# Optimization experiments

Measured on AMD Instinct MI355X. Metric: run time of the kernel, lower is better.

## Reference

```python
import jax, jax.numpy as jnp
import numpy as np

B, T, C = 4, 768, 2048
HEAD_SIZE = 64
H = C // HEAD_SIZE
D_W, D_A, D_MV, D_G = 96, 96, 64, 256
GN_EPS = 1e-5 * 8 ** 2  # head_size_divisor = 8


def _layer_norm(x, w, b, eps=1e-5):
    m = jnp.mean(x, -1, keepdims=True)
    v = jnp.mean(jnp.square(x - m), -1, keepdims=True)
    return (x - m) * jax.lax.rsqrt(v + eps) * w + b


def _time_shift(x):
    # ZeroPad2d((0,0,1,-1)): prepend a zero timestep, drop the last
    return jnp.pad(x, ((0, 0), (1, 0), (0, 0)))[:, :-1]


def _group_norm(x, w, b, eps):
    # x: [M, C], H groups
    M, Cc = x.shape
    xg = x.reshape(M, H, Cc // H)
    m = jnp.mean(xg, -1, keepdims=True)
    v = jnp.mean(jnp.square(xg - m), -1, keepdims=True)
    xg = (xg - m) * jax.lax.rsqrt(v + eps)
    return xg.reshape(M, Cc) * w + b


def _rwkv7(r, w, k, v, a, b):
    # WindBackstepping semantics: S_t = S_{t-1} * diag(exp(-exp(w_t))) + S_{t-1} a_t b_t^T + v_t k_t^T
    # y_t = S_t r_t ; state S is [B,H,N(v),N(k)]
    Bb, Tt, Cc = r.shape
    N = HEAD_SIZE
    r, w, k, v, a, b = [t.reshape(Bb, Tt, H, N) for t in (r, w, k, v, a, b)]
    decay = jnp.exp(-jnp.exp(w))  # [B,T,H,N]
    seq = tuple(jnp.moveaxis(t, 1, 0) for t in (decay, r, k, v, a, b))  # [T,B,H,N]
    s0 = jnp.zeros((Bb, H, N, N), jnp.float32)

    def step(s, inp):
        d_t, r_t, k_t, v_t, a_t, b_t = inp
        sab = jnp.einsum('bhik,bhk,bhj->bhij', s, a_t, b_t)
        s = s * d_t[:, :, None, :] + sab + v_t[..., :, None] * k_t[..., None, :]
        y_t = jnp.einsum('bhij,bhj->bhi', s, r_t)
        return s, y_t

    _, y = jax.lax.scan(step, s0, seq)
    return jnp.moveaxis(y, 0, 1).reshape(Bb, Tt, Cc)


def setup_inputs() -> dict:
    key = jax.random.key(0)
    ks = iter(jax.random.split(key, 48))
    rn = lambda shape, s=1.0: jax.random.normal(next(ks), shape, jnp.float32) * s
    d = {}
    d['x'] = rn((B, T, C))
    d['v_first'] = rn((B, T, C))
    d['ln1_w'] = jnp.ones((C,)); d['ln1_b'] = jnp.zeros((C,))
    d['ln2_w'] = jnp.ones((C,)); d['ln2_b'] = jnp.zeros((C,))
    ddd = jnp.arange(C, dtype=jnp.float32) / C
    for nm, p in [('x_r', 0.2), ('x_w', 0.9), ('x_k', 0.9), ('x_v', 0.4), ('x_a', 0.9), ('x_g', 0.2)]:
        d[nm] = 1.0 - jnp.power(ddd, p)
    d['w0'] = jnp.linspace(-7.0, -2.0, C) + 0.5
    d['w1'] = rn((C, D_W), 0.01); d['w2'] = rn((D_W, C), 0.02)
    d['a0'] = rn((C,), 0.1); d['a1'] = rn((C, D_A), 0.01); d['a2'] = rn((D_A, C), 0.02)
    d['v0'] = 1.0 + rn((C,), 0.1); d['v1'] = rn((C, D_MV), 0.01); d['v2'] = rn((D_MV, C), 0.02)
    d['g1'] = rn((C, D_G), 0.01); d['g2'] = rn((D_G, C), 0.02)
    d['k_k'] = 0.85 * jnp.ones((C,)); d['k_a'] = jnp.ones((C,))
    d['r_k'] = rn((H, HEAD_SIZE), 0.1)
    d['W_r'] = rn((C, C), C ** -0.5)
    d['W_k'] = rn((C, C), C ** -0.5)
    d['W_v'] = rn((C, C), C ** -0.5)
    d['W_o'] = rn((C, C), C ** -0.5)
    d['gn_w'] = jnp.ones((C,)); d['gn_b'] = jnp.zeros((C,))
    d['ffn_x_k'] = 1.0 - ddd
    d['W_key'] = rn((C, 4 * C), C ** -0.5)
    d['W_val'] = rn((4 * C, C), (4 * C) ** -0.5)
    return d


def reference(x, v_first, ln1_w, ln1_b, ln2_w, ln2_b, x_r, x_w, x_k, x_v, x_a, x_g,
              w0, w1, w2, a0, a1, a2, v0, v1, v2, g1, g2, k_k, k_a, r_k,
              W_r, W_k, W_v, W_o, gn_w, gn_b, ffn_x_k, W_key, W_val):
    N = HEAD_SIZE
    # ---- time mix (RWKV_Tmix_x070, layer_id=1) ----
    xn = _layer_norm(x, ln1_w, ln1_b)
    xx = _time_shift(xn) - xn
    xr = xn + xx * x_r
    xw_ = xn + xx * x_w
    xk_ = xn + xx * x_k
    xv_ = xn + xx * x_v
    xa_ = xn + xx * x_a
    xg_ = xn + xx * x_g
    r = xr @ W_r
    w_log = -jax.nn.softplus(-(w0 + jnp.tanh(xw_ @ w1) @ w2)) - 0.5
    k = xk_ @ W_k
    v = xv_ @ W_v
    v = v + (v_first - v) * jax.nn.sigmoid(v0 + (xv_ @ v1) @ v2)  # layer_id != 0
    a = jax.nn.sigmoid(a0 + (xa_ @ a1) @ a2)
    g = jax.nn.sigmoid(xg_ @ g1) @ g2
    kk = (k * k_k).reshape(B, T, H, N)
    kk = kk / jnp.maximum(jnp.linalg.norm(kk, axis=-1, keepdims=True), 1e-12)
    kk = kk.reshape(B, T, C)
    k = k * (1.0 + (a - 1.0) * k_a)
    y = _rwkv7(r, w_log, k, v, -kk, kk * a)
    y = _group_norm(y.reshape(B * T, C), gn_w, gn_b, GN_EPS).reshape(B, T, C)
    rk = jnp.sum(r.reshape(B, T, H, N) * k.reshape(B, T, H, N) * r_k, -1, keepdims=True)
    y = y + (rk * v.reshape(B, T, H, N)).reshape(B, T, C)
    x = x + (y * g) @ W_o
    # ---- channel mix (RWKV_CMix_x070) ----
    x2 = _layer_norm(x, ln2_w, ln2_b)
    xx2 = _time_shift(x2) - x2
    kf = x2 + xx2 * ffn_x_k
    kf = jnp.square(jax.nn.relu(kf @ W_key))
    x = x + kf @ W_val
    return (x, v_first)
```

## Files before the change

### kernel.cpp

```cpp
#include <hip/hip_runtime.h>
#include <stdint.h>

typedef unsigned short u16;
typedef __attribute__((ext_vector_type(8))) short short8;
typedef __attribute__((ext_vector_type(4))) float f32x4;

#define DEVI __device__ __forceinline__

static constexpr int TT = 768;
static constexpr int CC = 2048;
static constexpr int MM = 3072;
static constexpr int HH = 32;

DEVI float b2f(u16 u){ union{float f; unsigned int i;} x; x.i = ((unsigned int)u)<<16; return x.f; }
DEVI float b2fs(short s){ return b2f((u16)s); }
DEVI u16 f2b(float f){
  unsigned int u = __builtin_bit_cast(unsigned int, f);
  unsigned int r = (u + 0x7fffu + ((u>>16)&1u)) >> 16;
  return (u16)r;
}

DEVI void gload16(const void* g, void* s){
  __builtin_amdgcn_global_load_lds((const __attribute__((address_space(1))) void*)g,
                                   (__attribute__((address_space(3))) void*)s, 16, 0, 0);
}

__global__ __launch_bounds__(256) void k_fillf(float* __restrict__ out, float v, int n){
  for (int i = blockIdx.x*256 + threadIdx.x; i < n; i += gridDim.x*256) out[i] = v;
}

__global__ void k_tpose(const float* __restrict__ src, int R, int Cn, u16* __restrict__ dst, int ldd){
  __shared__ float tile[32][33];
  int c0 = blockIdx.x*32, r0 = blockIdx.y*32;
  #pragma unroll
  for (int i=0;i<4;++i){
    int r = r0 + threadIdx.y + i*8, c = c0 + threadIdx.x;
    tile[threadIdx.y + i*8][threadIdx.x] = (r<R && c<Cn) ? src[(size_t)r*Cn + c] : 0.f;
  }
  __syncthreads();
  #pragma unroll
  for (int i=0;i<4;++i){
    int c = c0 + threadIdx.y + i*8, r = r0 + threadIdx.x;
    if (c<Cn && r<R) dst[(size_t)c*ldd + r] = f2b(tile[threadIdx.x][threadIdx.y + i*8]);
  }
}

__global__ __launch_bounds__(256) void k_lnb(const float* __restrict__ in, const float* __restrict__ w,
                                             const float* __restrict__ bias, u16* __restrict__ out){
  __shared__ float red[8];
  int m = blockIdx.x;
  const float* x = in + (size_t)m*CC;
  float v[8]; float s=0.f, ss=0.f;
  #pragma unroll
  for (int i=0;i<8;++i){ v[i] = x[threadIdx.x + i*256]; s += v[i]; ss += v[i]*v[i]; }
  #pragma unroll
  for (int o=32;o;o>>=1){ s += __shfl_xor(s,o); ss += __shfl_xor(ss,o); }
  int wid = threadIdx.x>>6;
  if ((threadIdx.x&63)==0){ red[wid]=s; red[4+wid]=ss; }
  __syncthreads();
  s  = red[0]+red[1]+red[2]+red[3];
  ss = red[4]+red[5]+red[6]+red[7];
  float mean = s*(1.f/2048.f);
  float var  = ss*(1.f/2048.f) - mean*mean;
  float rstd = rsqrtf(fmaxf(var,0.f) + 1e-5f);
  #pragma unroll
  for (int i=0;i<8;++i){
    int c = threadIdx.x + i*256;
    out[(size_t)m*CC + c] = f2b((v[i]-mean)*rstd*w[c] + bias[c]);
  }
}

__global__ __launch_bounds__(256) void k_mixA(const u16* __restrict__ xn,
  const float* __restrict__ cw, const float* __restrict__ ca, const float* __restrict__ cv,
  const float* __restrict__ cg,
  u16* __restrict__ ow, u16* __restrict__ oa, u16* __restrict__ ov, u16* __restrict__ og)
{
  int m = blockIdx.x; int t = m % TT;
  const u16* cur = xn + (size_t)m*CC;
  const u16* prv = cur - CC;
  bool has = (t>0);
  #pragma unroll
  for (int i=0;i<8;++i){
    int c = threadIdx.x + i*256;
    float xc = b2f(cur[c]);
    float xx = (has ? b2f(prv[c]) : 0.f) - xc;
    size_t o = (size_t)m*CC + c;
    ow[o]=f2b(xc + xx*cw[c]); oa[o]=f2b(xc + xx*ca[c]);
    ov[o]=f2b(xc + xx*cv[c]); og[o]=f2b(xc + xx*cg[c]);
  }
}

__global__ __launch_bounds__(256) void k_mixB(const u16* __restrict__ xn,
  const float* __restrict__ cr, const float* __restrict__ ck,
  u16* __restrict__ orr, u16* __restrict__ ok)
{
  int m = blockIdx.x; int t = m % TT;
  const u16* cur = xn + (size_t)m*CC;
  const u16* prv = cur - CC;
  bool has = (t>0);
  #pragma unroll
  for (int i=0;i<8;++i){
    int c = threadIdx.x + i*256;
    float xc = b2f(cur[c]);
    float xx = (has ? b2f(prv[c]) : 0.f) - xc;
    size_t o = (size_t)m*CC + c;
    orr[o]=f2b(xc + xx*cr[c]); ok[o]=f2b(xc + xx*ck[c]);
  }
}

__global__ __launch_bounds__(256) void k_mix1(const u16* __restrict__ xn, const float* __restrict__ cf,
                                              u16* __restrict__ out){
  int m = blockIdx.x; int t = m % TT;
  const u16* cur = xn + (size_t)m*CC;
  const u16* prv = cur - CC;
  bool has = (t>0);
  #pragma unroll
  for (int i=0;i<8;++i){
    int c = threadIdx.x + i*256;
    float xc = b2f(cur[c]);
    float xx = (has ? b2f(prv[c]) : 0.f) - xc;
    out[(size_t)m*CC + c] = f2b(xc + xx*cf[c]);
  }
}

__global__ __launch_bounds__(256,2) void k_gemm(
    const u16* A0, const u16* A1, const u16* A2,
    int amode, int lda,
    const u16* __restrict__ BT, int ldb,
    void* C0, void* C1, void* C2, int ldc, int K,
    int emode, const float* __restrict__ aux)
{
  const int tid = threadIdx.x;
  const int w = tid>>6, l = tid&63;

  const int NT = gridDim.x;
  const int nwg = NT * gridDim.y;
  int bid = blockIdx.y * NT + blockIdx.x;
  int qq = nwg >> 3, rr = nwg & 7;
  int xcd = bid & 7, pos = bid >> 3;
  int nid = (xcd < rr ? xcd*(qq+1) : rr*(qq+1) + (xcd-rr)*qq) + pos;
  const int ntile = nid % NT;
  const int mtile = nid / NT;

  const u16* A = A0;
  if (amode==1){ A = (ntile==0)?A0:(ntile==1)?A1:A2; }
  else if (amode==2){ int g = ntile>>4; A = (g==0)?A0:(g==1)?A1:A2; }

  __shared__ __align__(16) u16 As[3*4096];
  __shared__ __align__(16) u16 Bs[3*4096];

  const int sr = w*16 + (l>>2);
  const int sk = (l&3)*8;
  const u16* Ag = A  + (size_t)(mtile*128 + sr)*lda + sk;
  const u16* Bg = BT + (size_t)(ntile*128 + sr)*ldb + sk;
  const size_t a64 = (size_t)64*lda, b64 = (size_t)64*ldb;
  const int wo = w*512;

  const int wm = w>>1, wn = w&1;
  const int fr = l&15, fk = (l>>4)*8;
  const int aoff = (wm*64 + fr)*32 + fk;
  const int boff = (wn*64 + fr)*32 + fk;

  f32x4 acc[4][4];
  const f32x4 zz = {0.f,0.f,0.f,0.f};
  #pragma unroll
  for (int mi=0;mi<4;++mi)
    #pragma unroll
    for (int ni=0;ni<4;++ni) acc[mi][ni] = zz;

  const int nt = K >> 5;

#define STAGE(bufi, k0) do{ \
    u16* dA = As + (bufi)*4096 + wo; \
    u16* dB = Bs + (bufi)*4096 + wo; \
    gload16(Ag + (k0),        dA); \
    gload16(Ag + a64 + (k0),  dA + 2048); \
    gload16(Bg + (k0),        dB); \
    gload16(Bg + b64 + (k0),  dB + 2048); \
  }while(0)

  STAGE(0, 0);
  if (nt > 1) STAGE(1, 32);

  int cur = 0;
  for (int t=0; t<nt; ++t){
    if (t == nt-1){ asm volatile("s_waitcnt vmcnt(0)" ::: "memory"); }
    else          { asm volatile("s_waitcnt vmcnt(4)" ::: "memory"); }
    __builtin_amdgcn_s_barrier();
    if (t+2 < nt){
      int nb = cur+2; if (nb>=3) nb-=3;
      STAGE(nb, (t+2)<<5);
    }
    const u16* Ab = As + cur*4096;
    const u16* Bb = Bs + cur*4096;
    short8 af[4], bfr[4];
    #pragma unroll
    for (int mi=0;mi<4;++mi) af[mi]  = *(const short8*)(Ab + aoff + mi*512);
    #pragma unroll
    for (int ni=0;ni<4;++ni) bfr[ni] = *(const short8*)(Bb + boff + ni*512);
    #pragma unroll
    for (int mi=0;mi<4;++mi)
      #pragma unroll
      for (int ni=0;ni<4;++ni)
        acc[mi][ni] = __builtin_amdgcn_mfma_f32_16x16x32_bf16(af[mi], bfr[ni], acc[mi][ni], 0,0,0);
    cur = (cur+1==3)?0:cur+1;
  }
#undef STAGE

  const int rb0 = mtile*128 + wm*64 + (l>>4)*4;
  const int cb0 = ntile*128 + wn*64 + fr;
  #pragma unroll
  for (int mi=0;mi<4;++mi){
    #pragma unroll
    for (int ni=0;ni<4;++ni){
      #pragma unroll
      for (int q2=0;q2<4;++q2){
        int row = rb0 + mi*16 + q2;
        int col = cb0 + ni*16;
        float v = acc[mi][ni][q2];
        if (emode==0){
          ((float*)C0)[(size_t)row*ldc + col] = v;
        } else if (emode==1){
          float valw = aux[col] + v;
          float zneg = -valw;
          float sp = (zneg > 20.f) ? zneg : log1pf(expf(zneg));
          float wlog = -sp - 0.5f;
          float dec = expf(-expf(wlog));
          int b_ = row/TT, t_ = row - b_*TT;
          int h_ = col>>6, n_ = col&63;
          ((float*)C0)[((size_t)(b_*HH + h_)*TT + t_)*64 + n_] = dec;
        } else if (emode==2){
          float s = 1.f/(1.f+expf(-(aux[col]+v)));
          ((u16*)C0)[(size_t)row*ldc + col] = f2b(s);
        } else if (emode==3){
          ((float*)C0)[(size_t)row*ldc + col] = aux[(size_t)row*ldc + col] + v;
        } else if (emode==4){
          float r_ = fmaxf(v, 0.f);
          ((u16*)C0)[(size_t)row*ldc + col] = f2b(r_*r_);
        } else if (emode==5){
          ((u16*)C0)[(size_t)row*ldc + col] = f2b(aux[(size_t)row*ldc + col] + v);
        } else if (emode==6){
          ((u16*)C0)[(size_t)row*ldc + col] = f2b(v);
        } else if (emode==7){
          float r_ = v;
          if (col < 128) r_ = tanhf(v);
          else if (col >= 384) r_ = 1.f/(1.f+expf(-v));
          ((u16*)C0)[(size_t)row*ldc + col] = f2b(r_);
        } else if (emode==8){
          int b_ = row/TT, t_ = row - b_*TT;
          int h_ = col>>6, n_ = col&63;
          ((u16*)C0)[((size_t)(b_*HH + h_)*TT + t_)*64 + n_] = f2b(v);
        } else if (emode==9){
          float s = 1.f/(1.f+expf(-(aux[col]+v)));
          int b_ = row/TT, t_ = row - b_*TT;
          int h_ = col>>6, n_ = col&63;
          ((u16*)C0)[((size_t)(b_*HH + h_)*TT + t_)*64 + n_] = f2b(s);
        } else if (emode==10){
          int g = col>>11, c2 = col&2047;
          int b_ = row/TT, t_ = row - b_*TT;
          int h_ = c2>>6, n_ = c2&63;
          u16* dst = (g==0)?(u16*)C0:(g==1)?(u16*)C1:(u16*)C2;
          dst[((size_t)(b_*HH + h_)*TT + t_)*64 + n_] = f2b(v);
        } else {
          float s = 1.f/(1.f+expf(-v));
          ((u16*)C0)[(size_t)row*ldc + (col+384)] = f2b(s);
        }
      }
    }
  }
}

__global__ __launch_bounds__(256) void k_make_rec3(
  u16* __restrict__ ksc, u16* __restrict__ vsc,
  const u16* __restrict__ asc, const u16* __restrict__ gsc,
  float* __restrict__ af, float* __restrict__ bf,
  const float* __restrict__ v_first, const float* __restrict__ k_k, const float* __restrict__ k_a)
{
  int idx = blockIdx.x*4 + (threadIdx.x>>6);
  int l = threadIdx.x & 63;
  int bh = idx / TT, t = idx - bh*TT;
  int b = bh >> 5, h = bh & 31;
  int c = h*64 + l;
  size_t off = (size_t)idx*64 + l;
  size_t mo = ((size_t)b*TT + t)*CC + c;
  float kq = b2f(ksc[off]);
  float vv = b2f(vsc[off]);
  float aa = b2f(asc[off]);
  float sg = b2f(gsc[off]);
  float vf = v_first[mo];
  float kkr = kq * k_k[c];
  float s2 = kkr*kkr;
  #pragma unroll
  for (int o=32;o;o>>=1) s2 += __shfl_xor(s2,o);
  float kk = kkr / fmaxf(sqrtf(s2), 1e-12f);
  ksc[off] = f2b(kq*(1.f + (aa-1.f)*k_a[c]));
  vsc[off] = f2b(vv + (vf-vv)*sg);
  af[off] = -kk;
  bf[off] = kk*aa;
}

struct StepB { f32x4 d[4]; f32x4 a[4]; f32x4 b[4]; short8 r[2], k[2]; float vi; };

DEVI void loadStep(StepB& sb, const float* __restrict__ dP, const float* __restrict__ aP,
                   const float* __restrict__ bP, const u16* __restrict__ rP,
                   const u16* __restrict__ kP, const u16* __restrict__ vP,
                   size_t off, size_t voff){
  const float* dp = dP + off;
  const float* ap = aP + off;
  const float* bp = bP + off;
  #pragma unroll
  for (int q=0;q<4;++q){
    sb.d[q] = *(const f32x4*)(dp+4*q);
    sb.a[q] = *(const f32x4*)(ap+4*q);
    sb.b[q] = *(const f32x4*)(bp+4*q);
  }
  const short8* rp = (const short8*)(rP + off);
  const short8* kp = (const short8*)(kP + off);
  sb.r[0]=rp[0]; sb.r[1]=rp[1];
  sb.k[0]=kp[0]; sb.k[1]=kp[1];
  sb.vi = b2f(vP[voff]);
}

DEVI float stepCompute(const StepB& sb, float S[16]){
  float sa = 0.f;
  #pragma unroll
  for (int q=0;q<16;++q) sa += S[q]*sb.a[q>>2][q&3];
  sa += __shfl_xor(sa,16); sa += __shfl_xor(sa,32);
  float yv = 0.f;
  #pragma unroll
  for (int q=0;q<16;++q){
    float Sq = S[q]*sb.d[q>>2][q&3] + sa*sb.b[q>>2][q&3] + sb.vi*b2fs(sb.k[q>>3][q&7]);
    S[q] = Sq;
    yv += Sq*b2fs(sb.r[q>>3][q&7]);
  }
  yv += __shfl_xor(yv,16); yv += __shfl_xor(yv,32);
  return yv;
}

__global__ __launch_bounds__(256,1) void k_rwkv(
    const float* __restrict__ decay, const float* __restrict__ af, const float* __restrict__ bf,
    const u16* __restrict__ rb, const u16* __restrict__ kb, const u16* __restrict__ vb,
    u16* __restrict__ y)
{
  int bh = blockIdx.x;
  int b = bh>>5, h = bh&31;
  int tid = threadIdx.x, w = tid>>6, l = tid&63;
  int i = w*16 + (l&15);
  int cch = l>>4;
  int j0 = cch*16;
  const size_t base = (size_t)bh * (TT*64);
  float S[16];
  #pragma unroll
  for (int q=0;q<16;++q) S[q]=0.f;

  size_t yb = (size_t)b*TT*CC + h*64 + i;
  StepB sA, sB;
  loadStep(sA, decay, af, bf, rb, kb, vb, base + j0, base + i);
  for (int t=0;t<TT;t+=2){
    loadStep(sB, decay, af, bf, rb, kb, vb, base + (size_t)(t+1)*64 + j0, base + (size_t)(t+1)*64 + i);
    float y0 = stepCompute(sA, S);
    if (cch==0) y[yb + (size_t)t*CC] = f2b(y0);
    if (t+2 < TT)
      loadStep(sA, decay, af, bf, rb, kb, vb, base + (size_t)(t+2)*64 + j0, base + (size_t)(t+2)*64 + i);
    float y1 = stepCompute(sB, S);
    if (cch==0) y[yb + (size_t)(t+1)*CC] = f2b(y1);
  }
}

__global__ __launch_bounds__(256) void k_gn(
  const u16* __restrict__ y, const u16* __restrict__ rb, const u16* __restrict__ kb,
  const u16* __restrict__ vb, const float* __restrict__ r_k,
  const float* __restrict__ gnw, const float* __restrict__ gnb,
  const u16* __restrict__ gg, u16* __restrict__ z)
{
  int idx = blockIdx.x*4 + (threadIdx.x>>6);
  int l = threadIdx.x&63;
  int m = idx>>5, h = idx&31;
  int c = h*64 + l;
  size_t mo = (size_t)m*CC + c;
  float yv = b2f(y[mo]);
  float s = yv;
  #pragma unroll
  for (int o=32;o;o>>=1) s += __shfl_xor(s,o);
  float mean = s*(1.f/64.f);
  float dv = yv - mean;
  float vs = dv*dv;
  #pragma unroll
  for (int o=32;o;o>>=1) vs += __shfl_xor(vs,o);
  float gn = dv*rsqrtf(vs*(1.f/64.f) + 6.4e-4f)*gnw[c] + gnb[c];
  size_t ro = ((size_t)((m/TT)*HH + h)*TT + (m%TT))*64 + l;
  float rv=b2f(rb[ro]), kv=b2f(kb[ro]), vv=b2f(vb[ro]);
  float p = rv*kv*r_k[c];
  #pragma unroll
  for (int o=32;o;o>>=1) p += __shfl_xor(p,o);
  z[mo] = f2b((gn + p*vv)*b2f(gg[mo]));
}

extern "C" void kernel_launch(void* const* d_in, const int* in_sizes, int n_in,
                              void* d_out, int out_size, void* d_ws, size_t ws_size,
                              hipStream_t stream)
{
  (void)out_size;
  const float* x      = (const float*)d_in[0];
  const float* v_first= (const float*)d_in[1];
  const float* ln1_w  = (const float*)d_in[2];
  const float* ln1_b  = (const float*)d_in[3];
  const float* ln2_w  = (const float*)d_in[4];
  const float* ln2_b  = (const float*)d_in[5];
  const float* x_r    = (const float*)d_in[6];
  const float* x_w    = (const float*)d_in[7];
  const float* x_k    = (const float*)d_in[8];
  const float* x_v    = (const float*)d_in[9];
  const float* x_a    = (const float*)d_in[10];
  const float* x_g    = (const float*)d_in[11];
  const float* w0     = (const float*)d_in[12];
  const float* w1     = (const float*)d_in[13];
  const float* w2     = (const float*)d_in[14];
  const float* a0     = (const float*)d_in[15];
  const float* a1     = (const float*)d_in[16];
  const float* a2     = (const float*)d_in[17];
  const float* v0     = (const float*)d_in[18];
  const float* v1     = (const float*)d_in[19];
  const float* v2     = (const float*)d_in[20];
  const float* g1     = (const float*)d_in[21];
  const float* g2     = (const float*)d_in[22];
  const float* k_k    = (const float*)d_in[23];
  const float* k_a    = (const float*)d_in[24];
  const float* r_k    = (const float*)d_in[25];
  const float* W_r    = (const float*)d_in[26];
  const float* W_k    = (const float*)d_in[27];
  const float* W_v    = (const float*)d_in[28];
  const float* W_o    = (const float*)d_in[29];
  const float* gn_w   = (const float*)d_in[30];
  const float* gn_b   = (const float*)d_in[31];
  const float* ffn_x_k= (const float*)d_in[32];
  const float* W_key  = (const float*)d_in[33];
  const float* W_val  = (const float*)d_in[34];

  const size_t ME = (size_t)MM*CC;
  float* outF = (float*)d_out;

  bool ok = (n_in==35)
    && in_sizes[0]==6291456 && in_sizes[1]==6291456 && in_sizes[2]==2048
    && in_sizes[12]==2048 && in_sizes[13]==196608 && in_sizes[14]==196608
    && in_sizes[16]==196608 && in_sizes[19]==131072 && in_sizes[21]==524288
    && in_sizes[25]==2048 && in_sizes[26]==4194304 && in_sizes[33]==16777216
    && in_sizes[34]==16777216;
  if (!ok){
    k_fillf<<<2048, 256, 0, stream>>>(outF, 1099511627776.f, (int)ME);
    return;
  }

  constexpr size_t WS_NEED = 125829120 + 12582912;
  if (ws_size < WS_NEED){
    k_fillf<<<2048, 256, 0, stream>>>(outF, (float)(1u<<21) * (float)(ws_size>>20), (int)ME);
    return;
  }
  char* ws = (char*)d_ws;
  float* decay = (float*)(ws + 0);
  float* x1    = (float*)(ws + 0);
  u16* xn   = (u16*)(ws + 25165824);
  u16* WT   = (u16*)(ws + 25165824);
  float* bf32 = (float*)(ws + 25165824);
  u16* xw  = (u16*)(ws + 37748736);
  u16* xr  = (u16*)(ws + 37748736);
  u16* xn2 = (u16*)(ws + 37748736);
  float* af32 = (float*)(ws + 50331648);
  u16* xa  = (u16*)(ws + 50331648);
  u16* xk  = (u16*)(ws + 50331648);
  u16* xv  = (u16*)(ws + 62914560);
  u16* kf  = (u16*)(ws + 62914560);
  u16* xg  = (u16*)(ws + 75497472);
  u16* rsc = (u16*)(ws + 75497472);
  char* Fs = ws + 88080384;
  u16* B1T = (u16*)(Fs);
  u16* w2T = (u16*)(Fs + 2621440);
  u16* a2T = (u16*)(Fs + 3014656);
  u16* v2T = (u16*)(Fs + 3407872);
  u16* g2T = (u16*)(Fs + 3670016);
  u16* H1b = (u16*)(Fs + 4718592);
  u16* ksc = (u16*)(ws + 88080384);
  u16* asc = (u16*)(ws + 100663296);
  u16* ybuf= (u16*)(ws + 100663296);
  u16* gsc = (u16*)(ws + 113246208);
  u16* zbuf= (u16*)(ws + 113246208);
  u16* xcm = (u16*)(ws + 113246208);
  u16* WbigT = (u16*)(ws + 25165824);
  u16* outG = (u16*)(ws + 125829120);
  u16* vsc   = (u16*)d_out;
  u16* WrkvT = ((u16*)d_out) + ME;

  auto GEMM = [&](const u16* a0_, const u16* a1_, const u16* a2_,
                  int amode, int lda_, const u16* bt, int ldb_,
                  void* c0_, void* c1_, void* c2_, int ldc_,
                  int N_, int K_, int em, const float* aux_){
    k_gemm<<<dim3(N_/128, MM/128), 256, 0, stream>>>(a0_,a1_,a2_,amode,lda_,bt,ldb_,c0_,c1_,c2_,ldc_,K_,em,aux_);
  };
  dim3 tb(32,8);

  k_lnb<<<MM, 256, 0, stream>>>(x, ln1_w, ln1_b, xn);
  k_mixA<<<MM, 256, 0, stream>>>(xn, x_w, x_a, x_v, x_g, xw, xa, xv, xg);
  hipMemsetAsync(B1T, 0, 2621440, stream);
  k_tpose<<<dim3(3,64), tb, 0, stream>>>(w1, 2048,  96, B1T + 0*2048,   2048);
  k_tpose<<<dim3(3,64), tb, 0, stream>>>(a1, 2048,  96, B1T + 128*2048, 2048);
  k_tpose<<<dim3(2,64), tb, 0, stream>>>(v1, 2048,  64, B1T + 256*2048, 2048);
  k_tpose<<<dim3(8,64), tb, 0, stream>>>(g1, 2048, 256, B1T + 384*2048, 2048);
  k_tpose<<<dim3(64,3), tb, 0, stream>>>(w2,   96, 2048, w2T,  96);
  k_tpose<<<dim3(64,3), tb, 0, stream>>>(a2,   96, 2048, a2T,  96);
  k_tpose<<<dim3(64,2), tb, 0, stream>>>(v2,   64, 2048, v2T,  64);
  k_tpose<<<dim3(64,8), tb, 0, stream>>>(g2,  256, 2048, g2T, 256);
  GEMM(xw, xa, xv, 1, 2048, B1T, 2048, H1b, nullptr, nullptr, 640, 384, 2048, 7, nullptr);
  GEMM(xg, xg, xg, 0, 2048, B1T + 384*2048, 2048, H1b, nullptr, nullptr, 640, 256, 2048, 11, nullptr);
  GEMM(H1b + 0,   H1b, H1b, 0, 640, w2T,  96, decay, nullptr, nullptr, 2048, 2048,  96, 1, w0);
  GEMM(H1b + 128, H1b, H1b, 0, 640, a2T,  96, asc,   nullptr, nullptr, 2048, 2048,  96, 9, a0);
  GEMM(H1b + 256, H1b, H1b, 0, 640, v2T,  64, gsc,   nullptr, nullptr, 2048, 2048,  64, 9, v0);
  GEMM(H1b + 384, H1b, H1b, 0, 640, g2T, 256, outG,  nullptr, nullptr, 2048, 2048, 256, 6, nullptr);
  k_mixB<<<MM, 256, 0, stream>>>(xn, x_r, x_k, xr, xk);
  k_tpose<<<dim3(64,64), tb, 0, stream>>>(W_r, 2048, 2048, WrkvT,               2048);
  k_tpose<<<dim3(64,64), tb, 0, stream>>>(W_k, 2048, 2048, WrkvT + 2048*2048,   2048);
  k_tpose<<<dim3(64,64), tb, 0, stream>>>(W_v, 2048, 2048, WrkvT + 2*2048*2048, 2048);
  GEMM(xr, xk, xv, 2, 2048, WrkvT, 2048, rsc, ksc, vsc, 2048, 6144, 2048, 10, nullptr);
  k_make_rec3<<<MM*HH/4, 256, 0, stream>>>(ksc, vsc, asc, gsc, af32, bf32, v_first, k_k, k_a);
  k_rwkv<<<128, 256, 0, stream>>>(decay, af32, bf32, rsc, ksc, vsc, ybuf);
  k_gn<<<MM*HH/4, 256, 0, stream>>>(ybuf, rsc, ksc, vsc, r_k, gn_w, gn_b, outG, zbuf);
  k_tpose<<<dim3(64,64), tb, 0, stream>>>(W_o, 2048, 2048, WT, 2048);
  GEMM(zbuf, zbuf, zbuf, 0, 2048, WT, 2048, x1, nullptr, nullptr, 2048, 2048, 2048, 3, x);
  k_lnb<<<MM, 256, 0, stream>>>(x1, ln2_w, ln2_b, xn2);
  k_mix1<<<MM, 256, 0, stream>>>(xn2, ffn_x_k, xcm);
  k_tpose<<<dim3(256,64), tb, 0, stream>>>(W_key, 2048, 8192, WbigT, 2048);
  GEMM(xcm, xcm, xcm, 0, 2048, WbigT, 2048, kf, nullptr, nullptr, 8192, 8192, 2048, 4, nullptr);
  k_tpose<<<dim3(64,256), tb, 0, stream>>>(W_val, 8192, 2048, WbigT, 8192);
  GEMM(kf, kf, kf, 0, 8192, WbigT, 8192, outF, nullptr, nullptr, 2048, 2048, 8192, 3, x1);
  hipMemcpyAsync(outF + ME, v_first, ME*sizeof(float), hipMemcpyDeviceToDevice, stream);
}
```

Before: 1.684 ms.

## Stage RWKV recurrence inputs through triple-buffered LDS chunks with async global loads

```diff
diff --git a/kernel.cpp b/kernel.cpp
--- a/kernel.cpp
+++ b/kernel.cpp
@@ -299,71 +299,117 @@
   bf[off] = kk*aa;
 }
 
-struct StepB { f32x4 d[4]; f32x4 a[4]; f32x4 b[4]; short8 r[2], k[2]; float vi; };
-
-DEVI void loadStep(StepB& sb, const float* __restrict__ dP, const float* __restrict__ aP,
-                   const float* __restrict__ bP, const u16* __restrict__ rP,
-                   const u16* __restrict__ kP, const u16* __restrict__ vP,
-                   size_t off, size_t voff){
-  const float* dp = dP + off;
-  const float* ap = aP + off;
-  const float* bp = bP + off;
-  #pragma unroll
-  for (int q=0;q<4;++q){
-    sb.d[q] = *(const f32x4*)(dp+4*q);
-    sb.a[q] = *(const f32x4*)(ap+4*q);
-    sb.b[q] = *(const f32x4*)(bp+4*q);
-  }
-  const short8* rp = (const short8*)(rP + off);
-  const short8* kp = (const short8*)(kP + off);
-  sb.r[0]=rp[0]; sb.r[1]=rp[1];
-  sb.k[0]=kp[0]; sb.k[1]=kp[1];
-  sb.vi = b2f(vP[voff]);
-}
-
-DEVI float stepCompute(const StepB& sb, float S[16]){
-  float sa = 0.f;
-  #pragma unroll
-  for (int q=0;q<16;++q) sa += S[q]*sb.a[q>>2][q&3];
-  sa += __shfl_xor(sa,16); sa += __shfl_xor(sa,32);
-  float yv = 0.f;
-  #pragma unroll
-  for (int q=0;q<16;++q){
-    float Sq = S[q]*sb.d[q>>2][q&3] + sa*sb.b[q>>2][q&3] + sb.vi*b2fs(sb.k[q>>3][q&7]);
-    S[q] = Sq;
-    yv += Sq*b2fs(sb.r[q>>3][q&7]);
-  }
-  yv += __shfl_xor(yv,16); yv += __shfl_xor(yv,32);
-  return yv;
-}
+static constexpr int RCH = 16;
+static constexpr int RNC = TT / RCH;
+static constexpr int RBUF = 18432;
 
 __global__ __launch_bounds__(256,1) void k_rwkv(
     const float* __restrict__ decay, const float* __restrict__ af, const float* __restrict__ bf,
     const u16* __restrict__ rb, const u16* __restrict__ kb, const u16* __restrict__ vb,
     u16* __restrict__ y)
 {
+  __shared__ __align__(16) char lds[3*RBUF];
   int bh = blockIdx.x;
   int b = bh>>5, h = bh&31;
   int tid = threadIdx.x, w = tid>>6, l = tid&63;
   int i = w*16 + (l&15);
-  int cch = l>>4;
-  int j0 = cch*16;
+  int j0 = (l>>4)*16;
   const size_t base = (size_t)bh * (TT*64);
+
+  const float* dB = decay + base;
+  const float* aB = af + base;
+  const float* bB = bf + base;
+  const u16*  rB = rb + base;
+  const u16*  kB = kb + base;
+  const u16*  vB = vb + base;
+
   float S[16];
   #pragma unroll
   for (int q=0;q<16;++q) S[q]=0.f;
-
+  float ycur[RCH], yprev[RCH];
   size_t yb = (size_t)b*TT*CC + h*64 + i;
-  StepB sA, sB;
-  loadStep(sA, decay, af, bf, rb, kb, vb, base + j0, base + i);
-  for (int t=0;t<TT;t+=2){
-    loadStep(sB, decay, af, bf, rb, kb, vb, base + (size_t)(t+1)*64 + j0, base + (size_t)(t+1)*64 + i);
-    float y0 = stepCompute(sA, S);
-    if (cch==0) y[yb + (size_t)t*CC] = f2b(y0);
-    if (t+2 < TT)
-      loadStep(sA, decay, af, bf, rb, kb, vb, base + (size_t)(t+2)*64 + j0, base + (size_t)(t+2)*64 + i);
-    float y1 = stepCompute(sB, S);
-    if (cch==0) y[yb + (size_t)(t+1)*CC] = f2b(y1);
+
+  const int fe = tid*4;
+  const int he = w*256 + l*8;
+  const bool hlo = (l < 32);
+
+#define RSTAGE(bufi, c) do{ \
+    char* bs = lds + (bufi)*RBUF; \
+    size_t cb = (size_t)(c)*1024; \
+    gload16(dB + cb + fe, bs + tid*16); \
+    gload16(aB + cb + fe, bs + 4096 + tid*16); \
+    gload16(bB + cb + fe, bs + 8192 + tid*16); \
+    if (hlo){ \
+      gload16(rB + cb + he, bs + 12288 + w*512 + l*16); \
+      gload16(kB + cb + he, bs + 14336 + w*512 + l*16); \
+      gload16(vB + cb + he, bs + 16384 + w*512 + l*16); \
+    } \
+  }while(0)
+
+  RSTAGE(0, 0);
+  RSTAGE(1, 1);
+
+  int cur = 0;
+  for (int c=0; c<RNC; ++c){
+    if (c == RNC-1){ asm volatile("s_waitcnt vmcnt(0)" ::: "memory"); }
+    else           { asm volatile("s_waitcnt vmcnt(6)" ::: "memory"); }
+    __builtin_amdgcn_s_barrier();
+    if (c > 0){
+      int t0 = (c-1)*RCH;
+      #pragma unroll
+      for (int s=0;s<RCH;++s) y[yb + (size_t)(t0+s)*CC] = f2b(yprev[s]);
+    }
+    asm volatile("" ::: "memory");
+    if (c+2 < RNC){
+      int nb = cur+2; if (nb>=3) nb-=3;
+      RSTAGE(nb, c+2);
+    }
+    asm volatile("" ::: "memory");
+    const char* bs = lds + cur*RBUF;
+    #pragma unroll
+    for (int s=0;s<RCH;++s){
+      const f32x4* aV = (const f32x4*)(bs + 4096 + s*256 + j0*4);
+      float sa = 0.f;
+      #pragma unroll
+      for (int q=0;q<4;++q){
+        f32x4 aq = aV[q];
+        #pragma unroll
+        for (int e=0;e<4;++e) sa += S[q*4+e]*aq[e];
+      }
+      sa += __shfl_xor(sa,16); sa += __shfl_xor(sa,32);
+      const f32x4* dV = (const f32x4*)(bs + s*256 + j0*4);
+      const f32x4* bV = (const f32x4*)(bs + 8192 + s*256 + j0*4);
+      const short8* rV = (const short8*)(bs + 12288 + s*128 + j0*2);
+      const short8* kV = (const short8*)(bs + 14336 + s*128 + j0*2);
+      float vi = b2f(*(const u16*)(bs + 16384 + s*128 + i*2));
+      short8 r0 = rV[0], r1 = rV[1];
+      short8 k0 = kV[0], k1 = kV[1];
+      float yv = 0.f;
+      #pragma unroll
+      for (int q=0;q<4;++q){
+        f32x4 dq = dV[q], bq = bV[q];
+        #pragma unroll
+        for (int e=0;e<4;++e){
+          const int idx = q*4+e;
+          float kk = b2fs(idx<8 ? k0[idx] : k1[idx-8]);
+          float rr = b2fs(idx<8 ? r0[idx] : r1[idx-8]);
+          float Sq = S[idx]*dq[e] + sa*bq[e] + vi*kk;
+          S[idx] = Sq;
+          yv += Sq*rr;
+        }
+      }
+      yv += __shfl_xor(yv,16); yv += __shfl_xor(yv,32);
+      ycur[s] = yv;
+    }
+    #pragma unroll
+    for (int s=0;s<RCH;++s) yprev[s] = ycur[s];
+    cur = (cur+1==3)?0:cur+1;
+  }
+#undef RSTAGE
+  {
+    int t0 = (RNC-1)*RCH;
+    #pragma unroll
+    for (int s=0;s<RCH;++s) y[yb + (size_t)(t0+s)*CC] = f2b(yprev[s]);
   }
 }
 
```

Result: faster. 1.551 ms (-7.9%).
